# Optimization experiments

Measured on AMD Instinct MI355X. Metric: run time of the kernel, lower is better.

The kernel has to match this reference:

```python
import jax, jax.numpy as jnp
import numpy as np

NUM_HEAD = 12
D_MODEL = 768
SEQ_LEN = 4096
D_K = D_MODEL // NUM_HEAD
NEG = -1e9  # matches masked_fill(-1000000000.0)


def setup_inputs() -> dict:
    key = jax.random.key(0)
    ks = jax.random.split(key, 9)
    s = 1.0 / np.sqrt(D_MODEL)
    inp = {
        "x": jax.random.normal(ks[0], (1, SEQ_LEN, D_MODEL), jnp.float32),
        "Wq": jax.random.normal(ks[1], (D_MODEL, D_MODEL), jnp.float32) * s,
        "bq": jax.random.normal(ks[2], (D_MODEL,), jnp.float32) * 0.01,
        "Wk": jax.random.normal(ks[3], (D_MODEL, D_MODEL), jnp.float32) * s,
        "bk": jax.random.normal(ks[4], (D_MODEL,), jnp.float32) * 0.01,
        "Wv": jax.random.normal(ks[5], (D_MODEL, D_MODEL), jnp.float32) * s,
        "bv": jax.random.normal(ks[6], (D_MODEL,), jnp.float32) * 0.01,
        "Wo": jax.random.normal(ks[7], (D_MODEL, D_MODEL), jnp.float32) * s,
        "bo": jax.random.normal(ks[8], (D_MODEL,), jnp.float32) * 0.01,
    }
    return inp


def reference(x, Wq, bq, Wk, bk, Wv, bv, Wo, bo):
    # x: [B, S, D]. nn.Linear computes x @ W.T + b.
    B, S, D = x.shape

    def proj(W, b):
        y = jnp.einsum("bsd,ed->bse", x, W) + b
        # [B, S, H, d_k] -> [B, H, S, d_k]
        return y.reshape(B, S, NUM_HEAD, D_K).transpose(0, 2, 1, 3)

    q = proj(Wq, bq)
    k = proj(Wk, bk)
    v = proj(Wv, bv)

    scores = jnp.einsum("bhqd,bhkd->bhqk", q, k) / jnp.sqrt(
        jnp.asarray(D_K, x.dtype)
    )
    # causal (subsequent) mask: position q attends to k <= q
    causal = jnp.tril(jnp.ones((S, S), bool))
    scores = jnp.where(causal[None, None], scores, jnp.asarray(NEG, x.dtype))
    p_attn = jax.nn.softmax(scores, axis=-1)  # dropout is identity in eval
    ctx = jnp.einsum("bhqk,bhkd->bhqd", p_attn, v)
    ctx = ctx.transpose(0, 2, 1, 3).reshape(B, S, D)
    return jnp.einsum("bsd,ed->bse", ctx, Wo) + bo
```

## Files before the change

### kernel.cpp

```cpp
#include <hip/hip_runtime.h>

#define SEQ 4096
#define DM  768
#define NH  12
#define DK  64

typedef __bf16 bf16_t;
typedef bf16_t bf16x8 __attribute__((ext_vector_type(8)));
typedef bf16_t bf16x4 __attribute__((ext_vector_type(4)));
typedef float  f32x4  __attribute__((ext_vector_type(4)));
typedef short  s16x4  __attribute__((ext_vector_type(4)));

#define LOG2E 1.44269504088896340736f
#define SM_C2 23.0831207f

static __device__ inline f32x4 mfma16x16x16_bf16(bf16x4 a, bf16x4 b, f32x4 c) {
#if __has_builtin(__builtin_amdgcn_mfma_f32_16x16x16_bf16)
    return __builtin_amdgcn_mfma_f32_16x16x16_bf16(a, b, c, 0, 0, 0);
#else
    return __builtin_amdgcn_mfma_f32_16x16x16bf16_1k(
        __builtin_bit_cast(s16x4, a), __builtin_bit_cast(s16x4, b), c, 0, 0, 0);
#endif
}

static __device__ __forceinline__ void gl_lds16(const bf16_t* g, bf16_t* l) {
    __builtin_amdgcn_global_load_lds(
        (const __attribute__((address_space(1))) void*)g,
        (__attribute__((address_space(3))) void*)l, 16, 0, 0);
}

__global__ __launch_bounds__(256) void cvt_bf16(
    const float* __restrict__ x,  const float* __restrict__ Wq,
    const float* __restrict__ Wk, const float* __restrict__ Wv,
    const float* __restrict__ Wo,
    bf16_t* __restrict__ xb, bf16_t* __restrict__ Wb)
{
    const int NXV = SEQ * DM / 4;
    const int NWV = DM * DM / 4;
    int i4 = blockIdx.x * 256 + threadIdx.x;
    const float* src; bf16_t* dst; int off;
    if (i4 < NXV) { src = x; dst = xb; off = i4; }
    else {
        int j = i4 - NXV;
        int w = j / NWV, jj = j - w * NWV;
        src = (w == 0) ? Wq : (w == 1) ? Wk : (w == 2) ? Wv : Wo;
        dst = Wb + (size_t)w * DM * DM;
        off = jj;
    }
    float4 v = *(const float4*)&src[(size_t)off * 4];
    bf16x4 t;
    t[0] = (bf16_t)v.x; t[1] = (bf16_t)v.y; t[2] = (bf16_t)v.z; t[3] = (bf16_t)v.w;
    *(bf16x4*)&dst[(size_t)off * 4] = t;
}

__global__ __launch_bounds__(256) void gemm_qkv2(
    const bf16_t* __restrict__ A, const bf16_t* __restrict__ Wb,
    const float* __restrict__ bq, const float* __restrict__ bk,
    const float* __restrict__ bv,
    bf16_t* __restrict__ Qb, bf16_t* __restrict__ Kb, bf16_t* __restrict__ Vbt)
{
    const int z = blockIdx.z;
    const bf16_t* W = Wb + (size_t)z * DM * DM;
    const float* bias = (z == 0) ? bq : (z == 1) ? bk : bv;

    __shared__ bf16_t As[128][64];
    __shared__ bf16_t Bs[128][64];

    const int tid  = threadIdx.x;
    const int wave = tid >> 6;
    const int lane = tid & 63;
    const int wm   = wave & 1, wn = wave >> 1;
    const int lrow = lane & 15;
    const int quad = lane >> 4;
    const int row0 = blockIdx.x * 128;
    const int col0 = blockIdx.y * 128;

    const int srow   = lane >> 3;
    const int schunk = (lane & 7) ^ srow;
    const int swz    = lrow & 7;

    f32x4 acc[4][4];
    #pragma unroll
    for (int i = 0; i < 4; i++)
        #pragma unroll
        for (int j = 0; j < 4; j++)
            acc[i][j] = (f32x4){0.f, 0.f, 0.f, 0.f};

    for (int k0 = 0; k0 < DM; k0 += 64) {
        __syncthreads();
        #pragma unroll
        for (int u = 0; u < 4; u++) {
            int R0 = wave * 32 + u * 8;
            gl_lds16(&A[(size_t)(row0 + R0 + srow) * DM + k0 + schunk * 8],
                     &As[R0][0]);
            gl_lds16(&W[(size_t)(col0 + R0 + srow) * DM + k0 + schunk * 8],
                     &Bs[R0][0]);
        }
        __syncthreads();

        #pragma unroll
        for (int s = 0; s < 2; s++) {
            bf16x8 af[4], bfr[4];
            #pragma unroll
            for (int mt = 0; mt < 4; mt++)
                af[mt] = *(const bf16x8*)
                    &As[wm * 64 + mt * 16 + lrow][(((s << 2) | quad) ^ swz) * 8];
            #pragma unroll
            for (int nt = 0; nt < 4; nt++)
                bfr[nt] = *(const bf16x8*)
                    &Bs[wn * 64 + nt * 16 + lrow][(((s << 2) | quad) ^ swz) * 8];
            #pragma unroll
            for (int mt = 0; mt < 4; mt++)
                #pragma unroll
                for (int nt = 0; nt < 4; nt++)
                    acc[mt][nt] = __builtin_amdgcn_mfma_f32_16x16x32_bf16(
                        af[mt], bfr[nt], acc[mt][nt], 0, 0, 0);
        }
    }

    if (z == 2) {
        #pragma unroll
        for (int nt = 0; nt < 4; nt++) {
            int col = col0 + wn * 64 + nt * 16 + lrow;
            float bvv = bias[col];
            #pragma unroll
            for (int mt = 0; mt < 4; mt++) {
                int row = row0 + wm * 64 + mt * 16 + quad * 4;
                bf16x4 t;
                #pragma unroll
                for (int r = 0; r < 4; r++) t[r] = (bf16_t)(acc[mt][nt][r] + bvv);
                *(bf16x4*)&Vbt[(size_t)col * SEQ + row] = t;
            }
        }
    } else {
        bf16_t* Cout = (z == 0) ? Qb : Kb;
        float scale = (z == 1) ? (0.125f * LOG2E) : 1.0f;
        #pragma unroll
        for (int nt = 0; nt < 4; nt++) {
            int col = col0 + wn * 64 + nt * 16 + lrow;
            float bvv = bias[col];
            #pragma unroll
            for (int mt = 0; mt < 4; mt++) {
                #pragma unroll
                for (int r = 0; r < 4; r++) {
                    int row = row0 + wm * 64 + mt * 16 + quad * 4 + r;
                    Cout[(size_t)row * DM + col] =
                        (bf16_t)((acc[mt][nt][r] + bvv) * scale);
                }
            }
        }
    }
}

__global__ __launch_bounds__(256) void gemm_out2(
    const bf16_t* __restrict__ A, const bf16_t* __restrict__ W,
    const float* __restrict__ bias, float* __restrict__ C)
{
    __shared__ bf16_t As[128][64];
    __shared__ bf16_t Bs[64][64];

    const int tid  = threadIdx.x;
    const int wave = tid >> 6;
    const int lane = tid & 63;
    const int wm   = wave & 1, wn = wave >> 1;
    const int lrow = lane & 15;
    const int quad = lane >> 4;
    const int row0 = blockIdx.x * 128;
    const int col0 = blockIdx.y * 64;

    const int srow   = lane >> 3;
    const int schunk = (lane & 7) ^ srow;
    const int swz    = lrow & 7;

    f32x4 acc[4][2];
    #pragma unroll
    for (int i = 0; i < 4; i++)
        #pragma unroll
        for (int j = 0; j < 2; j++)
            acc[i][j] = (f32x4){0.f, 0.f, 0.f, 0.f};

    for (int k0 = 0; k0 < DM; k0 += 64) {
        __syncthreads();
        #pragma unroll
        for (int u = 0; u < 4; u++) {
            int R0 = wave * 32 + u * 8;
            gl_lds16(&A[(size_t)(row0 + R0 + srow) * DM + k0 + schunk * 8],
                     &As[R0][0]);
        }
        #pragma unroll
        for (int u = 0; u < 2; u++) {
            int R0 = wave * 16 + u * 8;
            gl_lds16(&W[(size_t)(col0 + R0 + srow) * DM + k0 + schunk * 8],
                     &Bs[R0][0]);
        }
        __syncthreads();

        #pragma unroll
        for (int s = 0; s < 2; s++) {
            bf16x8 af[4], bfr[2];
            #pragma unroll
            for (int mt = 0; mt < 4; mt++)
                af[mt] = *(const bf16x8*)
                    &As[wm * 64 + mt * 16 + lrow][(((s << 2) | quad) ^ swz) * 8];
            #pragma unroll
            for (int nt = 0; nt < 2; nt++)
                bfr[nt] = *(const bf16x8*)
                    &Bs[wn * 32 + nt * 16 + lrow][(((s << 2) | quad) ^ swz) * 8];
            #pragma unroll
            for (int mt = 0; mt < 4; mt++)
                #pragma unroll
                for (int nt = 0; nt < 2; nt++)
                    acc[mt][nt] = __builtin_amdgcn_mfma_f32_16x16x32_bf16(
                        af[mt], bfr[nt], acc[mt][nt], 0, 0, 0);
        }
    }

    #pragma unroll
    for (int nt = 0; nt < 2; nt++) {
        int col = col0 + wn * 32 + nt * 16 + lrow;
        float bvv = bias[col];
        #pragma unroll
        for (int mt = 0; mt < 4; mt++) {
            #pragma unroll
            for (int r = 0; r < 4; r++) {
                int row = row0 + wm * 64 + mt * 16 + quad * 4 + r;
                C[(size_t)row * DM + col] = acc[mt][nt][r] + bvv;
            }
        }
    }
}

__global__ __launch_bounds__(256) void flash_split7(
    const bf16_t* __restrict__ Qb, const bf16_t* __restrict__ Kb,
    const bf16_t* __restrict__ Vbt,
    float* __restrict__ Oacc ,
    float* __restrict__ Lacc )
{
    const int h = blockIdx.z;
    const int f = 287 - blockIdx.x;
    int g = 0;
    while (f >= 4 * (g + 1) * (g + 2)) g++;
    const int rem = f - 4 * g * (g + 1);
    const int qs  = rem / (g + 1);
    const int seg = rem - qs * (g + 1);
    const int qi  = g * 8 + qs;
    const int q0  = qi << 6;
    const int kt0    = seg << 3;
    const int ktlast = min(kt0 + 7, qi);

    const int tid  = threadIdx.x;
    const int wave = tid >> 6;
    const int lane = tid & 63;
    const int lrow = lane & 15;
    const int quad = lane >> 4;
    const int swz  = lrow & 7;

    __shared__ bf16_t Ks[2][64][64];
    __shared__ bf16_t Vs[2][64][64];

    const int qrow = q0 + wave * 16 + lrow;
    bf16x8 qfrag[2];
    #pragma unroll
    for (int s = 0; s < 2; s++)
        qfrag[s] = *(const bf16x8*)&Qb[(size_t)qrow * DM + h * DK + s * 32 + quad * 8];

    f32x4 oT[4];
    #pragma unroll
    for (int dt = 0; dt < 4; dt++) oT[dt] = (f32x4){0.f, 0.f, 0.f, 0.f};
    float l_i = 0.f;

    const int srow8 = lane >> 3;
    const int schnk = (lane & 7) ^ srow8;

    size_t ko = (size_t)kt0 << 6;
    const bf16_t* kp = Kb  + (ko + wave * 16 + srow8) * DM + h * DK + schnk * 8;
    const bf16_t* vp = Vbt + ((size_t)(h * DK + wave * 16 + srow8)) * SEQ
                           + ko + schnk * 8;

    #define STAGE(bb)                                                          \
        do {                                                                   \
            gl_lds16(kp,            &Ks[bb][wave * 16][0]);                    \
            gl_lds16(kp + 8 * DM,   &Ks[bb][wave * 16 + 8][0]);                \
            gl_lds16(vp,            &Vs[bb][wave * 16][0]);                    \
            gl_lds16(vp + 8 * SEQ,  &Vs[bb][wave * 16 + 8][0]);                \
            kp += 64 * DM;                                                     \
            vp += 64;                                                          \
        } while (0)

    STAGE(0);

    for (int kt = kt0; kt <= ktlast; kt++) {
        const int b = kt & 1;
        __syncthreads();
        if (kt < ktlast) STAGE(b ^ 1);

        f32x4 sc[4];
        #pragma unroll
        for (int mt = 0; mt < 4; mt++) {
            f32x4 a = (f32x4){0.f, 0.f, 0.f, 0.f};
            #pragma unroll
            for (int s = 0; s < 2; s++) {
                bf16x8 kf = *(const bf16x8*)
                    &Ks[b][mt * 16 + lrow][(((s << 2) | quad) ^ swz) * 8];
                a = __builtin_amdgcn_mfma_f32_16x16x32_bf16(kf, qfrag[s], a, 0, 0, 0);
            }
            sc[mt] = a;
        }

        if (kt == qi) {
            #pragma unroll
            for (int mt = 0; mt < 4; mt++)
                #pragma unroll
                for (int rr = 0; rr < 4; rr++)
                    if ((kt << 6) + mt * 16 + quad * 4 + rr > qrow)
                        sc[mt][rr] = -1e30f;
        }

        bf16x4 pf[4];
        float rsum = 0.f;
        #pragma unroll
        for (int mt = 0; mt < 4; mt++) {
            bf16x4 t;
            #pragma unroll
            for (int rr = 0; rr < 4; rr++) {
                float p = __builtin_amdgcn_exp2f(sc[mt][rr] - SM_C2);
                rsum += p;
                t[rr] = (bf16_t)p;
            }
            pf[mt] = t;
        }
        l_i += rsum;

        #pragma unroll
        for (int dt = 0; dt < 4; dt++)
            #pragma unroll
            for (int kb = 0; kb < 4; kb++) {
                int c16 = (kb * 2 + (quad >> 1)) ^ swz;
                bf16x4 vf = *(const bf16x4*)
                    &Vs[b][dt * 16 + lrow][c16 * 8 + (quad & 1) * 4];
                oT[dt] = mfma16x16x16_bf16(vf, pf[kb], oT[dt]);
            }
    }
    #undef STAGE

    #pragma unroll
    for (int dt = 0; dt < 4; dt++)
        #pragma unroll
        for (int rr = 0; rr < 4; rr++) {
            int d = dt * 16 + quad * 4 + rr;
            atomicAdd(&Oacc[((size_t)h * DK + d) * SEQ + qrow], oT[dt][rr]);
        }
    l_i += __shfl_xor(l_i, 16, 64);
    l_i += __shfl_xor(l_i, 32, 64);
    if (quad == 0)
        atomicAdd(&Lacc[(size_t)h * SEQ + qrow], l_i);
}

__global__ __launch_bounds__(256) void ctx_epilogue(
    const float* __restrict__ Oacc, const float* __restrict__ Lacc,
    bf16_t* __restrict__ Ctx)
{
    const int qt = blockIdx.x;
    const int h  = blockIdx.y;
    const int tid = threadIdx.x;
    __shared__ float T[64][65];

    #pragma unroll
    for (int i = 0; i < 4; i++) {
        int v  = tid + i * 256;
        int d  = v >> 4;
        int qv = v & 15;
        f32x4 o4 = *(const f32x4*)&Oacc[((size_t)h * DK + d) * SEQ + qt * 64 + qv * 4];
        f32x4 l4 = *(const f32x4*)&Lacc[(size_t)h * SEQ + qt * 64 + qv * 4];
        #pragma unroll
        for (int j = 0; j < 4; j++)
            T[qv * 4 + j][d] = o4[j] / l4[j];
    }
    __syncthreads();
    #pragma unroll
    for (int i = 0; i < 2; i++) {
        int v  = tid + i * 256;
        int q  = v >> 3;
        int c8 = v & 7;
        bf16x8 t;
        #pragma unroll
        for (int j = 0; j < 8; j++)
            t[j] = (bf16_t)T[q][c8 * 8 + j];
        *(bf16x8*)&Ctx[(size_t)(qt * 64 + q) * DM + h * DK + c8 * 8] = t;
    }
}

extern "C" void kernel_launch(void* const* d_in, const int* in_sizes, int n_in,
                              void* d_out, int out_size, void* d_ws, size_t ws_size,
                              hipStream_t stream) {
    const float* x  = (const float*)d_in[0];
    const float* Wq = (const float*)d_in[1];
    const float* bq = (const float*)d_in[2];
    const float* Wk = (const float*)d_in[3];
    const float* bk = (const float*)d_in[4];
    const float* Wv = (const float*)d_in[5];
    const float* bv = (const float*)d_in[6];
    const float* Wo = (const float*)d_in[7];
    const float* bo = (const float*)d_in[8];
    float* out = (float*)d_out;

    const size_t NX = (size_t)SEQ * DM;
    const size_t NW = (size_t)DM * DM;

    bf16_t* xb   = (bf16_t*)d_ws;
    bf16_t* Qb   = xb  + NX;
    bf16_t* Kb   = Qb  + NX;
    bf16_t* Vbt  = Kb  + NX;
    bf16_t* Wb   = Vbt + NX;
    float*  Oacc = (float*)(Wb + 4 * NW);
    float*  Lacc = Oacc + NX;
    bf16_t* Cx   = xb;

    int cvt_blocks = (int)((NX + 4 * NW) / 4 / 256);
    cvt_bf16<<<cvt_blocks, 256, 0, stream>>>(x, Wq, Wk, Wv, Wo, xb, Wb);
    hipMemsetAsync(Oacc, 0, (NX + (size_t)NH * SEQ) * 4, stream);

    dim3 g1(SEQ / 128, DM / 128, 3);
    gemm_qkv2<<<g1, 256, 0, stream>>>(xb, Wb, bq, bk, bv, Qb, Kb, Vbt);

    dim3 g2(288, 1, NH);
    flash_split7<<<g2, 256, 0, stream>>>(Qb, Kb, Vbt, Oacc, Lacc);

    dim3 g3(SEQ / 64, NH);
    ctx_epilogue<<<g3, 256, 0, stream>>>(Oacc, Lacc, Cx);

    dim3 g4(SEQ / 128, DM / 64);
    gemm_out2<<<g4, 256, 0, stream>>>(Cx, Wb + 3 * NW, bo, out);
}
```

Baseline: 204.0 us.

## Drop split-KV atomics and fuse normalization into a single-pass flash kernel

The split-KV attention kernel, which accumulated partial O and L with float atomics, is replaced by one block per 64-row query tile that walks the whole causal KV range. Each block normalizes its output by the row sum and writes bf16 context directly. This removes the memset of the accumulators, the separate epilogue kernel, the global atomics and the extra fp32 round trip. The cost is less parallelism (768 blocks instead of 3456) and more load imbalance, since the heaviest tiles now run 64 KV iterations serially.

```diff
diff --git a/kernel.cpp b/kernel.cpp
--- a/kernel.cpp
+++ b/kernel.cpp
@@ -230,23 +230,14 @@
     }
 }
 
-__global__ __launch_bounds__(256) void flash_split7(
+__global__ __launch_bounds__(256) void flash_fused10(
     const bf16_t* __restrict__ Qb, const bf16_t* __restrict__ Kb,
     const bf16_t* __restrict__ Vbt,
-    float* __restrict__ Oacc ,
-    float* __restrict__ Lacc )
+    bf16_t* __restrict__ Ctx )
 {
-    const int h = blockIdx.z;
-    const int f = 287 - blockIdx.x;
-    int g = 0;
-    while (f >= 4 * (g + 1) * (g + 2)) g++;
-    const int rem = f - 4 * g * (g + 1);
-    const int qs  = rem / (g + 1);
-    const int seg = rem - qs * (g + 1);
-    const int qi  = g * 8 + qs;
-    const int q0  = qi << 6;
-    const int kt0    = seg << 3;
-    const int ktlast = min(kt0 + 7, qi);
+    const int h  = blockIdx.z;
+    const int qi = 63 - (int)blockIdx.x;
+    const int q0 = qi << 6;
 
     const int tid  = threadIdx.x;
     const int wave = tid >> 6;
@@ -272,27 +263,25 @@
     const int srow8 = lane >> 3;
     const int schnk = (lane & 7) ^ srow8;
 
-    size_t ko = (size_t)kt0 << 6;
-    const bf16_t* kp = Kb  + (ko + wave * 16 + srow8) * DM + h * DK + schnk * 8;
-    const bf16_t* vp = Vbt + ((size_t)(h * DK + wave * 16 + srow8)) * SEQ
-                           + ko + schnk * 8;
+    const bf16_t* kp = Kb  + (size_t)(wave * 16 + srow8) * DM + h * DK + schnk * 8;
+    const bf16_t* vp = Vbt + (size_t)(h * DK + wave * 16 + srow8) * SEQ + schnk * 8;
 
     #define STAGE(bb)                                                          \
         do {                                                                   \
-            gl_lds16(kp,            &Ks[bb][wave * 16][0]);                    \
-            gl_lds16(kp + 8 * DM,   &Ks[bb][wave * 16 + 8][0]);                \
-            gl_lds16(vp,            &Vs[bb][wave * 16][0]);                    \
-            gl_lds16(vp + 8 * SEQ,  &Vs[bb][wave * 16 + 8][0]);                \
+            gl_lds16(kp,           &Ks[bb][wave * 16][0]);                     \
+            gl_lds16(kp + 8 * DM,  &Ks[bb][wave * 16 + 8][0]);                 \
+            gl_lds16(vp,           &Vs[bb][wave * 16][0]);                     \
+            gl_lds16(vp + 8 * SEQ, &Vs[bb][wave * 16 + 8][0]);                 \
             kp += 64 * DM;                                                     \
             vp += 64;                                                          \
         } while (0)
 
     STAGE(0);
 
-    for (int kt = kt0; kt <= ktlast; kt++) {
+    for (int kt = 0; kt <= qi; kt++) {
         const int b = kt & 1;
         __syncthreads();
-        if (kt < ktlast) STAGE(b ^ 1);
+        if (kt < qi) STAGE(b ^ 1);
 
         f32x4 sc[4];
         #pragma unroll
@@ -343,50 +332,16 @@
     }
     #undef STAGE
 
-    #pragma unroll
-    for (int dt = 0; dt < 4; dt++)
-        #pragma unroll
-        for (int rr = 0; rr < 4; rr++) {
-            int d = dt * 16 + quad * 4 + rr;
-            atomicAdd(&Oacc[((size_t)h * DK + d) * SEQ + qrow], oT[dt][rr]);
-        }
     l_i += __shfl_xor(l_i, 16, 64);
     l_i += __shfl_xor(l_i, 32, 64);
-    if (quad == 0)
-        atomicAdd(&Lacc[(size_t)h * SEQ + qrow], l_i);
-}
-
-__global__ __launch_bounds__(256) void ctx_epilogue(
-    const float* __restrict__ Oacc, const float* __restrict__ Lacc,
-    bf16_t* __restrict__ Ctx)
-{
-    const int qt = blockIdx.x;
-    const int h  = blockIdx.y;
-    const int tid = threadIdx.x;
-    __shared__ float T[64][65];
-
-    #pragma unroll
-    for (int i = 0; i < 4; i++) {
-        int v  = tid + i * 256;
-        int d  = v >> 4;
-        int qv = v & 15;
-        f32x4 o4 = *(const f32x4*)&Oacc[((size_t)h * DK + d) * SEQ + qt * 64 + qv * 4];
-        f32x4 l4 = *(const f32x4*)&Lacc[(size_t)h * SEQ + qt * 64 + qv * 4];
-        #pragma unroll
-        for (int j = 0; j < 4; j++)
-            T[qv * 4 + j][d] = o4[j] / l4[j];
-    }
-    __syncthreads();
-    #pragma unroll
-    for (int i = 0; i < 2; i++) {
-        int v  = tid + i * 256;
-        int q  = v >> 3;
-        int c8 = v & 7;
-        bf16x8 t;
-        #pragma unroll
-        for (int j = 0; j < 8; j++)
-            t[j] = (bf16_t)T[q][c8 * 8 + j];
-        *(bf16x8*)&Ctx[(size_t)(qt * 64 + q) * DM + h * DK + c8 * 8] = t;
+    float inv = 1.0f / l_i;
+
+    #pragma unroll
+    for (int dt = 0; dt < 4; dt++) {
+        bf16x4 t;
+        #pragma unroll
+        for (int rr = 0; rr < 4; rr++) t[rr] = (bf16_t)(oT[dt][rr] * inv);
+        *(bf16x4*)&Ctx[(size_t)qrow * DM + h * DK + dt * 16 + quad * 4] = t;
     }
 }
 
@@ -412,22 +367,16 @@
     bf16_t* Kb   = Qb  + NX;
     bf16_t* Vbt  = Kb  + NX;
     bf16_t* Wb   = Vbt + NX;
-    float*  Oacc = (float*)(Wb + 4 * NW);
-    float*  Lacc = Oacc + NX;
     bf16_t* Cx   = xb;
 
     int cvt_blocks = (int)((NX + 4 * NW) / 4 / 256);
     cvt_bf16<<<cvt_blocks, 256, 0, stream>>>(x, Wq, Wk, Wv, Wo, xb, Wb);
-    hipMemsetAsync(Oacc, 0, (NX + (size_t)NH * SEQ) * 4, stream);
 
     dim3 g1(SEQ / 128, DM / 128, 3);
     gemm_qkv2<<<g1, 256, 0, stream>>>(xb, Wb, bq, bk, bv, Qb, Kb, Vbt);
 
-    dim3 g2(288, 1, NH);
-    flash_split7<<<g2, 256, 0, stream>>>(Qb, Kb, Vbt, Oacc, Lacc);
-
-    dim3 g3(SEQ / 64, NH);
-    ctx_epilogue<<<g3, 256, 0, stream>>>(Oacc, Lacc, Cx);
+    dim3 g2(SEQ / 64, 1, NH);
+    flash_fused10<<<g2, 256, 0, stream>>>(Qb, Kb, Vbt, Cx);
 
     dim3 g4(SEQ / 128, DM / 64);
     gemm_out2<<<g4, 256, 0, stream>>>(Cx, Wb + 3 * NW, bo, out);
```

After: 213.1 us. 1.04x slower.
